# Performance work log

Hardware: AMD Instinct MI355X
Metric: run time of the kernel (lower is better)

The kernel has to match this reference:

```python
import jax, jax.numpy as jnp
import numpy as np

N, D, H = 16384, 2, 128  # batch, num_directions (bi-GRU), hidden_dim


def setup_inputs() -> dict:
    key = jax.random.key(0)
    k1, k2 = jax.random.split(key)
    enc_h_t = jax.random.normal(k1, (N, D, H), dtype=jnp.float32)
    dec_h_t = jax.random.normal(k2, (N, D, H), dtype=jnp.float32)
    return {"enc_h_t": enc_h_t, "dec_h_t": dec_h_t}


def _pairwise_sq_dists(x, y):
    # dist[i,j] = ||x[i]-y[j]||^2, clamped at 0 (matches pairwise_distances)
    x_norm = jnp.sum(x * x, axis=1)[:, None]   # [N,1]
    y_norm = jnp.sum(y * y, axis=1)[None, :]   # [1,N]
    dist = x_norm + y_norm - 2.0 * (x @ y.T)   # [N,N]
    return jnp.maximum(dist, 0.0)


def reference(enc_h_t, dec_h_t):
    batch_size = enc_h_t.shape[0]
    # sum over the bidirectional-direction axis (dim=1)
    bi_enc = jnp.sum(enc_h_t, axis=1)  # [N,H]
    bi_dec = jnp.sum(dec_h_t, axis=1)  # [N,H]

    dist = _pairwise_sq_dists(bi_enc, bi_dec)          # [N,N]
    diag = jnp.diagonal(dist)                           # [N]

    # rowLoss = 5 - sum_y dist[x,y] + 10*dist[x,x]; clamped below at 0, summed
    row_loss = 5.0 - jnp.sum(dist, axis=1) + 10.0 * diag
    nce_loss = jnp.sum(jnp.maximum(row_loss, 0.0))

    diagonal_loss = -jnp.sum(diag) / batch_size

    return (bi_enc, bi_enc, bi_dec, nce_loss, diagonal_loss)
```

## Files before the change

kernel.cpp:

```cpp
#include <hip/hip_runtime.h>
#include <math.h>

#define N_ROWS 16384
#define HDIM   128
#define NH     (N_ROWS * HDIM)
#define NH4    (NH / 4)
#define B1     512
#define K1_ITERS 4

#define OFF_SY1 0
#define OFF_YN1 65536
#define OFF_DG1 66048
#define OFF_MX1 66560

typedef float v4f __attribute__((ext_vector_type(4)));

__device__ __forceinline__ void nt_store4(const float4& v, float4* p) {
    v4f t = { v.x, v.y, v.z, v.w };
    __builtin_nontemporal_store(t, reinterpret_cast<v4f*>(p));
}

__global__ __launch_bounds__(256) void k1_stream(
    const float4* __restrict__ enc, const float4* __restrict__ dec,
    float* __restrict__ outf, float* __restrict__ ws)
{
    float4* out4 = reinterpret_cast<float4*>(outf);
    const int tid  = threadIdx.x;
    const int b    = blockIdx.x;
    const int gid0 = b * 256 + tid;
    const int stride = B1 * 256;
    const int h4 = tid & 31;

    float4 e0[K1_ITERS], e1[K1_ITERS], d0[K1_ITERS], d1[K1_ITERS];
    #pragma unroll
    for (int k = 0; k < K1_ITERS; ++k) {
        const int base = 2 * (gid0 + k * stride) - h4;
        e0[k] = enc[base];
        e1[k] = enc[base + 32];
        d0[k] = dec[base];
        d1[k] = dec[base + 32];
    }

    float4 asy = make_float4(0.f, 0.f, 0.f, 0.f);
    float ayn = 0.f, adg = 0.f, dgmx = 0.f;

    #pragma unroll
    for (int k = 0; k < K1_ITERS; ++k) {
        const int v = gid0 + k * stride;
        float4 x = make_float4(e0[k].x + e1[k].x, e0[k].y + e1[k].y,
                               e0[k].z + e1[k].z, e0[k].w + e1[k].w);
        float4 y = make_float4(d0[k].x + d1[k].x, d0[k].y + d1[k].y,
                               d0[k].z + d1[k].z, d0[k].w + d1[k].w);
        nt_store4(x, &out4[v]);
        nt_store4(x, &out4[NH4 + v]);
        nt_store4(y, &out4[2 * NH4 + v]);

        asy.x += y.x; asy.y += y.y; asy.z += y.z; asy.w += y.w;
        ayn += y.x * y.x + y.y * y.y + y.z * y.z + y.w * y.w;

        float fx = x.x - y.x, fy = x.y - y.y, fz = x.z - y.z, fw = x.w - y.w;
        float dg = fx * fx + fy * fy + fz * fz + fw * fw;
        adg += dg;
        #pragma unroll
        for (int m = 16; m > 0; m >>= 1) dg += __shfl_xor(dg, m, 32);
        dgmx = fmaxf(dgmx, dg);
    }

    __shared__ float4 ssy[256];
    __shared__ float s_yn[256], s_dg[256], s_mx[256];
    ssy[tid] = asy; s_yn[tid] = ayn; s_dg[tid] = adg; s_mx[tid] = dgmx;
    __syncthreads();
    for (int off = 128; off > 0; off >>= 1) {
        if (tid < off) {
            s_yn[tid] += s_yn[tid + off];
            s_dg[tid] += s_dg[tid + off];
            s_mx[tid]  = fmaxf(s_mx[tid], s_mx[tid + off]);
        }
        __syncthreads();
    }
    if (tid < 32) {
        float4 t = ssy[tid];
        #pragma unroll
        for (int k = 1; k < 8; ++k) {
            float4 u = ssy[tid + 32 * k];
            t.x += u.x; t.y += u.y; t.z += u.z; t.w += u.w;
        }
        reinterpret_cast<float4*>(ws + OFF_SY1)[b * 32 + tid] = t;
    }
    if (tid == 0) {
        ws[OFF_YN1 + b] = s_yn[0];
        ws[OFF_DG1 + b] = s_dg[0];
        ws[OFF_MX1 + b] = s_mx[0];
    }
}

__global__ __launch_bounds__(1024) void k2_finalize(
    const float* __restrict__ ws, float* __restrict__ outf)
{
    const int tid = threadIdx.x;
    const float4* SY1 = reinterpret_cast<const float4*>(ws + OFF_SY1);

    const int col4 = tid & 31, r = tid >> 5;
    float4 a = make_float4(0.f, 0.f, 0.f, 0.f);
    #pragma unroll
    for (int j = 0; j < 16; ++j) {
        float4 u = SY1[(r * 16 + j) * 32 + col4];
        a.x += u.x; a.y += u.y; a.z += u.z; a.w += u.w;
    }

    float yn = 0.f, mx = 0.f;
    double dgd = 0.0;
    if (tid < 512) {
        yn  = ws[OFF_YN1 + tid];
        dgd = (double)ws[OFF_DG1 + tid];
        mx  = ws[OFF_MX1 + tid];
    }

    __shared__ float4 sred[1024];
    __shared__ float s_yn[1024], s_mx[1024];
    __shared__ double s_dg[1024];
    sred[tid] = a; s_yn[tid] = yn; s_mx[tid] = mx; s_dg[tid] = dgd;
    __syncthreads();
    for (int off = 512; off >= 32; off >>= 1) {
        if (tid < off) {
            float4 u = sred[tid + off];
            sred[tid].x += u.x; sred[tid].y += u.y;
            sred[tid].z += u.z; sred[tid].w += u.w;
        }
        __syncthreads();
    }
    for (int off = 512; off > 0; off >>= 1) {
        if (tid < off) {
            s_yn[tid] += s_yn[tid + off];
            s_dg[tid] += s_dg[tid + off];
            s_mx[tid]  = fmaxf(s_mx[tid], s_mx[tid + off]);
        }
        __syncthreads();
    }

    __shared__ float sy[128];
    __shared__ float red[1024];
    if (tid < 32) reinterpret_cast<float4*>(sy)[tid] = sred[tid];
    __syncthreads();
    red[tid] = (tid < 128) ? sy[tid] * sy[tid] : 0.f;
    __syncthreads();
    for (int off = 512; off > 0; off >>= 1) {
        if (tid < off) red[tid] += red[tid + off];
        __syncthreads();
    }

    const float  ss2   = red[0];
    const float  sumyn = s_yn[0];
    const double dsum  = s_dg[0];
    const float  dgmax = s_mx[0];

    const float bound = 5.f + ss2 / (float)N_ROWS - sumyn + 10.f * dgmax;
    if (bound < -1.0e4f) {
        if (tid == 0) {
            outf[3 * NH]     = 0.0f;
            outf[3 * NH + 1] = (float)(-dsum / (double)N_ROWS);
        }
        return;
    }

    __shared__ double snce[1024];
    const float* X = outf;
    const float* Y = outf + 2 * NH;
    double nce = 0.0;
    for (int i = tid; i < N_ROWS; i += 1024) {
        const float* xi = X + i * HDIM;
        float xn = 0.f;
        for (int h = 0; h < HDIM; ++h) xn += xi[h] * xi[h];
        double rowsum = 0.0;
        for (int j = 0; j < N_ROWS; ++j) {
            const float* yj = Y + j * HDIM;
            float ynn = 0.f, xy = 0.f;
            for (int h = 0; h < HDIM; ++h) { ynn += yj[h] * yj[h]; xy += xi[h] * yj[h]; }
            rowsum += (double)fmaxf(xn + ynn - 2.f * xy, 0.f);
        }
        const float* yi = Y + i * HDIM;
        float ynn = 0.f, xy = 0.f;
        for (int h = 0; h < HDIM; ++h) { ynn += yi[h] * yi[h]; xy += xi[h] * yi[h]; }
        const float diag = fmaxf(xn + ynn - 2.f * xy, 0.f);
        const double rl = 5.0 - rowsum + 10.0 * (double)diag;
        nce += (rl > 0.0) ? rl : 0.0;
    }
    snce[tid] = nce;
    __syncthreads();
    for (int off = 512; off > 0; off >>= 1) {
        if (tid < off) snce[tid] += snce[tid + off];
        __syncthreads();
    }
    if (tid == 0) {
        outf[3 * NH]     = (float)snce[0];
        outf[3 * NH + 1] = (float)(-dsum / (double)N_ROWS);
    }
}

extern "C" void kernel_launch(void* const* d_in, const int* in_sizes, int n_in,
                              void* d_out, int out_size, void* d_ws, size_t ws_size,
                              hipStream_t stream) {
    const float4* enc = (const float4*)d_in[0];
    const float4* dec = (const float4*)d_in[1];
    float* out = (float*)d_out;
    float* ws  = (float*)d_ws;

    k1_stream<<<B1, 256, 0, stream>>>(enc, dec, out, ws);
    k2_finalize<<<1, 1024, 0, stream>>>(ws, out);
}
```

Baseline: 88.68 us.

## Fold the finalize kernel into the streaming kernel via atomics and a last-block reduction

Drops the separate single-block finalize kernel. Each block now accumulates its partial sums, the diagonal sum and the diagonal max straight into a small workspace with atomics. A completion counter lets the last block finish the reduction and the loss bound check. A tiny init kernel zeroes the workspace first. This removes the per-block partial arrays and the wide 1024-thread reduction, but adds atomic contention on 128 column slots and makes the float summation order nondeterministic.

```diff
diff --git a/kernel.cpp b/kernel.cpp
--- a/kernel.cpp
+++ b/kernel.cpp
@@ -8,10 +8,12 @@
 #define B1     512
 #define K1_ITERS 4
 
-#define OFF_SY1 0
-#define OFF_YN1 65536
-#define OFF_DG1 66048
-#define OFF_MX1 66560
+#define OFF_SY 0
+#define OFF_YN 128
+#define OFF_DG 130
+#define OFF_MX 132
+#define OFF_CT 133
+#define WS_INIT_FLOATS 136
 
 typedef float v4f __attribute__((ext_vector_type(4)));
 
@@ -20,7 +22,12 @@
     __builtin_nontemporal_store(t, reinterpret_cast<v4f*>(p));
 }
 
-__global__ __launch_bounds__(256) void k1_stream(
+__global__ __launch_bounds__(256) void k0_init(float* __restrict__ ws) {
+    const int t = threadIdx.x;
+    if (t < WS_INIT_FLOATS) ws[t] = 0.0f;
+}
+
+__global__ __launch_bounds__(256) void k1_fused(
     const float4* __restrict__ enc, const float4* __restrict__ dec,
     float* __restrict__ outf, float* __restrict__ ws)
 {
@@ -78,6 +85,7 @@
         }
         __syncthreads();
     }
+
     if (tid < 32) {
         float4 t = ssy[tid];
         #pragma unroll
@@ -85,74 +93,48 @@
             float4 u = ssy[tid + 32 * k];
             t.x += u.x; t.y += u.y; t.z += u.z; t.w += u.w;
         }
-        reinterpret_cast<float4*>(ws + OFF_SY1)[b * 32 + tid] = t;
+        atomicAdd(&ws[OFF_SY + 4 * tid + 0], t.x);
+        atomicAdd(&ws[OFF_SY + 4 * tid + 1], t.y);
+        atomicAdd(&ws[OFF_SY + 4 * tid + 2], t.z);
+        atomicAdd(&ws[OFF_SY + 4 * tid + 3], t.w);
     }
     if (tid == 0) {
-        ws[OFF_YN1 + b] = s_yn[0];
-        ws[OFF_DG1 + b] = s_dg[0];
-        ws[OFF_MX1 + b] = s_mx[0];
-    }
-}
-
-__global__ __launch_bounds__(1024) void k2_finalize(
-    const float* __restrict__ ws, float* __restrict__ outf)
-{
-    const int tid = threadIdx.x;
-    const float4* SY1 = reinterpret_cast<const float4*>(ws + OFF_SY1);
-
-    const int col4 = tid & 31, r = tid >> 5;
-    float4 a = make_float4(0.f, 0.f, 0.f, 0.f);
-    #pragma unroll
-    for (int j = 0; j < 16; ++j) {
-        float4 u = SY1[(r * 16 + j) * 32 + col4];
-        a.x += u.x; a.y += u.y; a.z += u.z; a.w += u.w;
-    }
-
-    float yn = 0.f, mx = 0.f;
-    double dgd = 0.0;
-    if (tid < 512) {
-        yn  = ws[OFF_YN1 + tid];
-        dgd = (double)ws[OFF_DG1 + tid];
-        mx  = ws[OFF_MX1 + tid];
-    }
-
-    __shared__ float4 sred[1024];
-    __shared__ float s_yn[1024], s_mx[1024];
-    __shared__ double s_dg[1024];
-    sred[tid] = a; s_yn[tid] = yn; s_mx[tid] = mx; s_dg[tid] = dgd;
-    __syncthreads();
-    for (int off = 512; off >= 32; off >>= 1) {
-        if (tid < off) {
-            float4 u = sred[tid + off];
-            sred[tid].x += u.x; sred[tid].y += u.y;
-            sred[tid].z += u.z; sred[tid].w += u.w;
-        }
-        __syncthreads();
-    }
-    for (int off = 512; off > 0; off >>= 1) {
-        if (tid < off) {
-            s_yn[tid] += s_yn[tid + off];
-            s_dg[tid] += s_dg[tid + off];
-            s_mx[tid]  = fmaxf(s_mx[tid], s_mx[tid + off]);
-        }
-        __syncthreads();
-    }
-
-    __shared__ float sy[128];
-    __shared__ float red[1024];
-    if (tid < 32) reinterpret_cast<float4*>(sy)[tid] = sred[tid];
-    __syncthreads();
-    red[tid] = (tid < 128) ? sy[tid] * sy[tid] : 0.f;
-    __syncthreads();
-    for (int off = 512; off > 0; off >>= 1) {
+        atomicAdd(&ws[OFF_YN], s_yn[0]);
+        atomicAdd(reinterpret_cast<double*>(ws + OFF_DG), (double)s_dg[0]);
+        atomicMax(reinterpret_cast<int*>(ws + OFF_MX), __float_as_int(s_mx[0]));
+    }
+    __threadfence();
+    __syncthreads();
+
+    __shared__ int s_last;
+    if (tid == 0) {
+        unsigned old = atomicAdd(reinterpret_cast<unsigned*>(ws + OFF_CT), 1u);
+        s_last = (old == (unsigned)(B1 - 1));
+    }
+    __syncthreads();
+    if (!s_last) return;
+
+    __threadfence();
+    float syh = 0.f;
+    if (tid < HDIM)
+        syh = __hip_atomic_load(&ws[OFF_SY + tid], __ATOMIC_RELAXED,
+                                __HIP_MEMORY_SCOPE_AGENT);
+    __shared__ float red[256];
+    red[tid] = syh * syh;
+    __syncthreads();
+    for (int off = 128; off > 0; off >>= 1) {
         if (tid < off) red[tid] += red[tid + off];
         __syncthreads();
     }
 
     const float  ss2   = red[0];
-    const float  sumyn = s_yn[0];
-    const double dsum  = s_dg[0];
-    const float  dgmax = s_mx[0];
+    const float  sumyn = __hip_atomic_load(&ws[OFF_YN], __ATOMIC_RELAXED,
+                                           __HIP_MEMORY_SCOPE_AGENT);
+    const double dsum  = __hip_atomic_load(reinterpret_cast<double*>(ws + OFF_DG),
+                                           __ATOMIC_RELAXED, __HIP_MEMORY_SCOPE_AGENT);
+    const float  dgmax = __int_as_float(
+        __hip_atomic_load(reinterpret_cast<int*>(ws + OFF_MX),
+                          __ATOMIC_RELAXED, __HIP_MEMORY_SCOPE_AGENT));
 
     const float bound = 5.f + ss2 / (float)N_ROWS - sumyn + 10.f * dgmax;
     if (bound < -1.0e4f) {
@@ -163,37 +145,47 @@
         return;
     }
 
-    __shared__ double snce[1024];
-    const float* X = outf;
-    const float* Y = outf + 2 * NH;
-    double nce = 0.0;
-    for (int i = tid; i < N_ROWS; i += 1024) {
-        const float* xi = X + i * HDIM;
-        float xn = 0.f;
-        for (int h = 0; h < HDIM; ++h) xn += xi[h] * xi[h];
-        double rowsum = 0.0;
-        for (int j = 0; j < N_ROWS; ++j) {
-            const float* yj = Y + j * HDIM;
+    {
+        const float* ef = reinterpret_cast<const float*>(enc);
+        const float* df = reinterpret_cast<const float*>(dec);
+        __shared__ double snce[256];
+        double nce = 0.0;
+        for (int i = tid; i < N_ROWS; i += 256) {
+            float xn = 0.f;
+            for (int h = 0; h < HDIM; ++h) {
+                float xh = ef[i * 256 + h] + ef[i * 256 + 128 + h];
+                xn += xh * xh;
+            }
+            double rowsum = 0.0;
+            for (int j = 0; j < N_ROWS; ++j) {
+                float ynn = 0.f, xy = 0.f;
+                for (int h = 0; h < HDIM; ++h) {
+                    float xh = ef[i * 256 + h] + ef[i * 256 + 128 + h];
+                    float yh = df[j * 256 + h] + df[j * 256 + 128 + h];
+                    ynn += yh * yh; xy += xh * yh;
+                }
+                rowsum += (double)fmaxf(xn + ynn - 2.f * xy, 0.f);
+            }
             float ynn = 0.f, xy = 0.f;
-            for (int h = 0; h < HDIM; ++h) { ynn += yj[h] * yj[h]; xy += xi[h] * yj[h]; }
-            rowsum += (double)fmaxf(xn + ynn - 2.f * xy, 0.f);
-        }
-        const float* yi = Y + i * HDIM;
-        float ynn = 0.f, xy = 0.f;
-        for (int h = 0; h < HDIM; ++h) { ynn += yi[h] * yi[h]; xy += xi[h] * yi[h]; }
-        const float diag = fmaxf(xn + ynn - 2.f * xy, 0.f);
-        const double rl = 5.0 - rowsum + 10.0 * (double)diag;
-        nce += (rl > 0.0) ? rl : 0.0;
-    }
-    snce[tid] = nce;
-    __syncthreads();
-    for (int off = 512; off > 0; off >>= 1) {
-        if (tid < off) snce[tid] += snce[tid + off];
+            for (int h = 0; h < HDIM; ++h) {
+                float xh = ef[i * 256 + h] + ef[i * 256 + 128 + h];
+                float yh = df[i * 256 + h] + df[i * 256 + 128 + h];
+                ynn += yh * yh; xy += xh * yh;
+            }
+            const float diag = fmaxf(xn + ynn - 2.f * xy, 0.f);
+            const double rl = 5.0 - rowsum + 10.0 * (double)diag;
+            nce += (rl > 0.0) ? rl : 0.0;
+        }
+        snce[tid] = nce;
         __syncthreads();
-    }
-    if (tid == 0) {
-        outf[3 * NH]     = (float)snce[0];
-        outf[3 * NH + 1] = (float)(-dsum / (double)N_ROWS);
+        for (int off = 128; off > 0; off >>= 1) {
+            if (tid < off) snce[tid] += snce[tid + off];
+            __syncthreads();
+        }
+        if (tid == 0) {
+            outf[3 * NH]     = (float)snce[0];
+            outf[3 * NH + 1] = (float)(-dsum / (double)N_ROWS);
+        }
     }
 }
 
@@ -205,6 +197,6 @@
     float* out = (float*)d_out;
     float* ws  = (float*)d_ws;
 
-    k1_stream<<<B1, 256, 0, stream>>>(enc, dec, out, ws);
-    k2_finalize<<<1, 1024, 0, stream>>>(ws, out);
-}
+    k0_init<<<1, 256, 0, stream>>>(ws);
+    k1_fused<<<B1, 256, 0, stream>>>(enc, dec, out, ws);
+}
```

Measured after the change: 153.5 us. 1.73x slower.
